# Optimization experiments

Measured on AMD Instinct MI355X. Metric: run time of the kernel, lower is better.

The kernel has to match this reference:

```python
import jax, jax.numpy as jnp
import numpy as np

HIDDEN = 2048
NUM_HEADS = 16
HEAD_DIM = HIDDEN // NUM_HEADS


def setup_inputs() -> dict:
    key = jax.random.key(0)
    k1, k2, k3 = jax.random.split(key, 3)
    B, S = 2, 2048
    hidden_states = jax.random.normal(k1, (B, S, HIDDEN), dtype=jnp.float32)
    attention_mask = jnp.zeros((B, 1, 1, S), dtype=jnp.float32)
    W_qkv = jax.random.normal(k2, (HIDDEN, 3 * HIDDEN), dtype=jnp.float32) * (1.0 / np.sqrt(HIDDEN))
    b_qkv = jnp.zeros((3 * HIDDEN,), dtype=jnp.float32)
    W_out = jax.random.normal(k3, (HIDDEN, HIDDEN), dtype=jnp.float32) * (1.0 / np.sqrt(HIDDEN))
    b_out = jnp.zeros((HIDDEN,), dtype=jnp.float32)
    return {"hidden_states": hidden_states, "attention_mask": attention_mask,
            "W_qkv": W_qkv, "b_qkv": b_qkv, "W_out": W_out, "b_out": b_out}


def reference(hidden_states, attention_mask, W_qkv, b_qkv, W_out, b_out):
    B, S, H = hidden_states.shape
    scale = 1.0 / np.sqrt(HEAD_DIM)
    # fused QKV projection (column-parallel linear, world_size=1)
    mixed = hidden_states @ W_qkv + b_qkv                      # [B,S,3H]
    q, k, v = jnp.split(mixed, 3, axis=-1)
    # [B, heads, S, head_dim]
    q = q.reshape(B, S, NUM_HEADS, HEAD_DIM).transpose(0, 2, 1, 3)
    k = k.reshape(B, S, NUM_HEADS, HEAD_DIM).transpose(0, 2, 1, 3)
    v = v.reshape(B, S, NUM_HEADS, HEAD_DIM).transpose(0, 2, 1, 3)
    scores = jnp.einsum('bhqd,bhkd->bhqk', q, k) * scale       # [B,h,S,S]
    scores = scores + attention_mask                            # additive mask broadcast
    probs = jax.nn.softmax(scores, axis=-1)
    ctx = jnp.einsum('bhqk,bhkd->bhqd', probs, v)               # [B,h,S,d]
    ctx = ctx.transpose(0, 2, 1, 3).reshape(B, S, H)
    return ctx @ W_out + b_out
```

## Files before the change

kernel.cpp:

```cpp
#include <hip/hip_runtime.h>
#include <hip/hip_bf16.h>
#include <stdint.h>

typedef __attribute__((ext_vector_type(4)))  float   f32x4;
typedef __attribute__((ext_vector_type(16))) float   f32x16;
typedef __attribute__((ext_vector_type(8)))  __bf16  bf16x8;
typedef __attribute__((ext_vector_type(8)))  short   s16x8;
typedef __attribute__((ext_vector_type(4)))  unsigned short u16x4;
typedef __attribute__((ext_vector_type(4)))  float   fl4;
typedef __attribute__((ext_vector_type(2)))  unsigned int u32x2;
typedef __attribute__((ext_vector_type(4)))  unsigned int u32x4;

#define DEVFN static __device__ __forceinline__

constexpr int BATCH = 2, SEQ = 2048, HID = 2048, NHEAD = 16, HDIM = 128;
constexpr int MROWS = BATCH * SEQ;
constexpr int N3    = 3 * HID;
constexpr float LOG2E = 1.44269504088896340736f;
constexpr float SCALE_LOG2E = 0.12751649736170852f;
constexpr float DEFER_THR = 11.541560327111708f;

DEVFN unsigned short f2bf(float f) {
  unsigned int u = __float_as_uint(f);
  u += 0x7FFFu + ((u >> 16) & 1u);
  return (unsigned short)(u >> 16);
}

DEVFN void async_cp16(const void* g, void* l) {
  __builtin_amdgcn_global_load_lds(
      (__attribute__((address_space(1))) void*)g,
      (__attribute__((address_space(3))) void*)l, 16, 0, 0);
}

DEVFN f32x4 mfma_bf16(bf16x8 a, bf16x8 b, f32x4 c) {
  return __builtin_amdgcn_mfma_f32_16x16x32_bf16(a, b, c, 0, 0, 0);
}
DEVFN f32x16 mfma32(bf16x8 a, bf16x8 b, f32x16 c) {
  return __builtin_amdgcn_mfma_f32_32x32x16_bf16(a, b, c, 0, 0, 0);
}
DEVFN unsigned cvt_pk_bf16(float lo, float hi) {
  unsigned r;
  asm("v_cvt_pk_bf16_f32 %0, %1, %2" : "=v"(r) : "v"(lo), "v"(hi));
  return r;
}

__global__ __launch_bounds__(256) void cvt_bf16(const float* __restrict__ x,
                                                unsigned short* __restrict__ hi, int n4) {
  for (int i = blockIdx.x * blockDim.x + threadIdx.x; i < n4; i += gridDim.x * blockDim.x) {
    fl4 v = ((const fl4*)x)[i];
    u16x4 h;
#pragma unroll
    for (int j = 0; j < 4; j++) h[j] = f2bf(v[j]);
    ((u16x4*)hi)[i] = h;
  }
}

__global__ __launch_bounds__(256) void cvt_transpose(const float* __restrict__ W,
                                                     unsigned short* __restrict__ T,
                                                     int R, int C) {
  __shared__ float tile[32][33];
  const int c0 = blockIdx.x * 32, r0 = blockIdx.y * 32;
  const int tx = threadIdx.x, ty = threadIdx.y;
#pragma unroll
  for (int i = 0; i < 4; i++) tile[ty + 8 * i][tx] = W[(size_t)(r0 + ty + 8 * i) * C + c0 + tx];
  __syncthreads();
#pragma unroll
  for (int i = 0; i < 4; i++) {
    const float v = tile[tx][ty + 8 * i];
    T[(size_t)(c0 + ty + 8 * i) * R + r0 + tx] = f2bf(v);
  }
}

template <bool OUT_BF16>
__global__ __launch_bounds__(512, 1) void gemm_ring(const unsigned short* __restrict__ A,
                                                    const unsigned short* __restrict__ Bt,
                                                    const float* __restrict__ bias,
                                                    void* __restrict__ Cout, int Ndim) {
  constexpr int KDIM  = 2048;
  constexpr int NT    = KDIM / 64;
  constexpr int ASLOT = 256 * 64;
  constexpr int BSLOT = 128 * 64;
  constexpr int SLOT  = ASLOT + BSLOT;
  __shared__ __align__(16) unsigned short smem[3 * SLOT];

  const int tid = threadIdx.x;
  const int wid = tid >> 6, lane = tid & 63;
  const int wm = wid >> 2, wn = wid & 3;
  const int g = lane >> 4, q = lane & 15;
  const int n0 = blockIdx.x * 128, m0 = blockIdx.y * 256;

  const int srow = (wid << 3) + (lane >> 3);
  const int scol = (((lane & 7) ^ (lane >> 3)) << 4);
  const char* gA = (const char*)A  + ((size_t)(m0 + srow) * KDIM) * 2 + scol;
  const char* gB = (const char*)Bt + ((size_t)(n0 + srow) * KDIM) * 2 + scol;
  const int dbase = ((wid << 3)) << 7;

  f32x4 acc[8][2] = {};
  const int axor = (q & 7) << 4;

  auto STAGE = [&](int tt, int slot) {
    char* sA = (char*)(smem + slot * SLOT);
    char* sB = (char*)(smem + slot * SLOT + ASLOT);
    const size_t koff = (size_t)tt << 7;
#pragma unroll
    for (int i = 0; i < 4; i++)
      async_cp16(gA + (size_t)(i * 64) * (KDIM * 2) + koff, sA + dbase + (i << 13));
#pragma unroll
    for (int i = 0; i < 2; i++)
      async_cp16(gB + (size_t)(i * 64) * (KDIM * 2) + koff, sB + dbase + (i << 13));
  };

  auto COMPUTE = [&](int slot) {
    const char* sA = (const char*)(smem + slot * SLOT);
    const char* sB = (const char*)(smem + slot * SLOT + ASLOT);
#pragma unroll
    for (int ks = 0; ks < 2; ks++) {
      const int kb = (ks << 6) + (g << 4);
      bf16x8 av[8], bv[2];
#pragma unroll
      for (int nf = 0; nf < 2; nf++) {
        const int row = (wn << 5) + (nf << 4) + q;
        bv[nf] = *(const bf16x8*)(sB + (row << 7) + (kb ^ axor));
      }
#pragma unroll
      for (int mf = 0; mf < 8; mf++) {
        const int row = (wm << 7) + (mf << 4) + q;
        av[mf] = *(const bf16x8*)(sA + (row << 7) + (kb ^ axor));
      }
#pragma unroll
      for (int mf = 0; mf < 8; mf++)
#pragma unroll
        for (int nf = 0; nf < 2; nf++)
          acc[mf][nf] = mfma_bf16(av[mf], bv[nf], acc[mf][nf]);
    }
  };

  STAGE(0, 0);
  STAGE(1, 1);
  int s2 = 2, sc = 0;
#pragma unroll 1
  for (int t = 0; t < NT - 2; ++t) {
    asm volatile("s_waitcnt vmcnt(6)" ::: "memory");
    __builtin_amdgcn_s_barrier();
    asm volatile("" ::: "memory");
    STAGE(t + 2, s2);
    COMPUTE(sc);
    s2 = (s2 == 2) ? 0 : s2 + 1;
    sc = (sc == 2) ? 0 : sc + 1;
  }
  asm volatile("s_waitcnt vmcnt(6)" ::: "memory");
  __builtin_amdgcn_s_barrier();
  asm volatile("" ::: "memory");
  COMPUTE(sc);
  sc = (sc == 2) ? 0 : sc + 1;
  asm volatile("s_waitcnt vmcnt(0)" ::: "memory");
  __builtin_amdgcn_s_barrier();
  asm volatile("" ::: "memory");
  COMPUTE(sc);

  float bvv[2];
#pragma unroll
  for (int nf = 0; nf < 2; nf++) bvv[nf] = bias[n0 + (wn << 5) + (nf << 4) + q];
#pragma unroll
  for (int mf = 0; mf < 8; mf++) {
    const int rowg = m0 + (wm << 7) + (mf << 4) + (g << 2);
#pragma unroll
    for (int nf = 0; nf < 2; nf++) {
      const int colg = n0 + (wn << 5) + (nf << 4) + q;
#pragma unroll
      for (int r = 0; r < 4; r++) {
        const float v = acc[mf][nf][r] + bvv[nf];
        if (OUT_BF16)
          ((unsigned short*)Cout)[(size_t)(rowg + r) * Ndim + colg] = f2bf(v);
        else
          ((float*)Cout)[(size_t)(rowg + r) * Ndim + colg] = v;
      }
    }
  }
}

__global__ __launch_bounds__(256) void transpose_v(const unsigned short* __restrict__ qkv,
                                                   unsigned short* __restrict__ vt) {
  __shared__ __align__(16) unsigned short tile[64][136];
  const int z = blockIdx.y, b = z >> 4, h = z & 15;
  const int s0 = blockIdx.x << 6;
  const int t = threadIdx.x;
#pragma unroll
  for (int i = 0; i < 4; i++) {
    const int idx = t + (i << 8);
    const int row = idx >> 4, ch = idx & 15;
    *(s16x8*)&tile[row][ch << 3] =
        *(const s16x8*)(qkv + (size_t)(b * SEQ + s0 + row) * N3 + 2 * HID + h * HDIM + (ch << 3));
  }
  __syncthreads();
#pragma unroll
  for (int i = 0; i < 4; i++) {
    const int idx = t + (i << 8);
    const int d = idx >> 3, sc = idx & 7;
    s16x8 v;
#pragma unroll
    for (int j = 0; j < 8; j++) v[j] = (short)tile[(sc << 3) + j][d];
    *(s16x8*)(vt + (size_t)(z * HDIM + d) * SEQ + s0 + (sc << 3)) = v;
  }
}

__global__ __launch_bounds__(256, 2) void attn_kernel(const unsigned short* __restrict__ qkv,
                                                      const unsigned short* __restrict__ vt,
                                                      const float* __restrict__ mask,
                                                      unsigned short* __restrict__ ctx) {
  constexpr int NT    = SEQ / 64;
  constexpr int KSLOT = 64 * 128;
  constexpr int VSLOT = 64 * 128;
  constexpr int SLOT  = KSLOT + VSLOT;
  __shared__ __align__(16) unsigned short sKV[2 * SLOT];
  __shared__ __align__(16) float sM[SEQ];

  const int bid = blockIdx.x;
  const int idx = bid >> 3;
  const int z  = ((bid & 7) << 2) + (idx >> 4);
  const int qb = idx & 15;
  const int b = z >> 4, h = z & 15;
  const int tid = threadIdx.x, wid = tid >> 6, lane = tid & 63;
  const int l31 = lane & 31, hi = lane >> 5;
  const int q0w = (qb << 7) + (wid << 5);

#pragma unroll
  for (int j = 0; j < 2; j++) {
    fl4 m = ((const fl4*)(mask + (size_t)b * SEQ))[tid + (j << 8)];
    m *= LOG2E;
    ((fl4*)sM)[tid + (j << 8)] = m;
  }

  bf16x8 bq[8];
  {
    const char* qrow = (const char*)(qkv + (size_t)(b * SEQ + q0w + l31) * N3 + h * HDIM);
#pragma unroll
    for (int kc = 0; kc < 8; kc++) bq[kc] = *(const bf16x8*)(qrow + (kc << 5) + (hi << 4));
  }

  f32x16 acc2[4] = {};
  float mrun = -1e30f, lrun = 0.f;

  const char* gK = (const char*)qkv + ((size_t)(b * SEQ) * N3 + HID + h * HDIM) * 2;
  const char* gV = (const char*)vt + ((size_t)z * HDIM * SEQ) * 2;

  auto STAGE = [&](int tt, int slot) {
    char* kb_ = (char*)(sKV + slot * SLOT);
    char* vb_ = kb_ + KSLOT * 2;
    const int k0 = tt << 6;
#pragma unroll
    for (int i = 0; i < 4; i++) {
      const int row = (i << 4) + (wid << 2) + (lane >> 4);
      const int sl  = lane & 15;
      const int dst = (i << 12) + (wid << 10);
      async_cp16(gK + ((size_t)(k0 + row) * N3) * 2 + (((sl ^ (row & 15))) << 4), kb_ + dst);
      const int sv  = sl ^ (row & 15);
      const int dhi = sv >> 3, kc8 = sv & 7;
      async_cp16(gV + ((size_t)((dhi << 6) + row) * SEQ + k0 + (kc8 << 3)) * 2, vb_ + dst);
    }
  };

  auto COMPUTE = [&](int t, int slot) {
    const char* sK = (const char*)(sKV + slot * SLOT);
    const char* sV = (const char*)(sKV + slot * SLOT + KSLOT);
    const int k0 = t << 6;

    f32x16 accs[2] = {};
    __builtin_amdgcn_s_setprio(1);
#pragma unroll
    for (int kb = 0; kb < 2; kb++)
#pragma unroll
      for (int kc = 0; kc < 8; kc++) {
        const int key = (kb << 5) + l31;
        const bf16x8 ka = *(const bf16x8*)(sK + (key << 8) +
                                           ((((kc << 1) + hi) ^ (l31 & 15)) << 4));
        accs[kb] = mfma32(ka, bq[kc], accs[kb]);
      }
    __builtin_amdgcn_s_setprio(0);

    float p_[2][16];
#pragma unroll
    for (int kb = 0; kb < 2; kb++) {
      fl4 mk[4];
#pragma unroll
      for (int m = 0; m < 4; m++) mk[m] = *(const fl4*)&sM[k0 + (kb << 5) + (m << 3) + (hi << 2)];
#pragma unroll
      for (int r = 0; r < 16; r++)
        p_[kb][r] = fmaf(accs[kb][r], SCALE_LOG2E, mk[r >> 2][r & 3]);
    }
    float mt = p_[0][0];
#pragma unroll
    for (int kb = 0; kb < 2; kb++)
#pragma unroll
      for (int r = 0; r < 16; r++) mt = fmaxf(mt, p_[kb][r]);
    mt = fmaxf(mt, __shfl_xor(mt, 32));
    if (!__all(mt <= mrun + DEFER_THR)) {
      const float mnew = fmaxf(mrun, mt);
      const float fs = exp2f(mrun - mnew);
      lrun *= fs;
#pragma unroll
      for (int r = 0; r < 16; r++) {
        const int qr = (r & 3) + ((r >> 2) << 3) + (hi << 2);
        const float fr = __shfl(fs, (lane & 32) | qr);
#pragma unroll
        for (int db = 0; db < 4; db++) acc2[db][r] *= fr;
      }
      mrun = mnew;
    }
    float ps = 0.f;
#pragma unroll
    for (int kb = 0; kb < 2; kb++)
#pragma unroll
      for (int r = 0; r < 16; r++) {
        const float e = exp2f(p_[kb][r] - mrun);
        p_[kb][r] = e;
        ps += e;
      }
    ps += __shfl_xor(ps, 32);
    lrun += ps;

    bf16x8 pa[4];
#pragma unroll
    for (int kb = 0; kb < 2; kb++)
#pragma unroll
      for (int hh = 0; hh < 2; hh++) {
        const float* pp = &p_[kb][hh << 3];
        const unsigned x01 = cvt_pk_bf16(pp[0], pp[1]);
        const unsigned x23 = cvt_pk_bf16(pp[2], pp[3]);
        const unsigned y01 = cvt_pk_bf16(pp[4], pp[5]);
        const unsigned y23 = cvt_pk_bf16(pp[6], pp[7]);
        const u32x2 sa = __builtin_amdgcn_permlane32_swap(x01, y01, false, false);
        const u32x2 sb = __builtin_amdgcn_permlane32_swap(x23, y23, false, false);
        const u32x4 w = {sa[0], sb[0], sa[1], sb[1]};
        pa[(kb << 1) + hh] = __builtin_bit_cast(bf16x8, w);
      }

    __builtin_amdgcn_s_setprio(1);
#pragma unroll
    for (int db = 0; db < 4; db++) {
      const int dd = ((db & 1) << 5) + l31;
#pragma unroll
      for (int ks = 0; ks < 4; ks++) {
        const int sv = ((db >> 1) << 3) + (ks << 1) + hi;
        const bf16x8 bv = *(const bf16x8*)(sV + (dd << 8) + ((sv ^ (l31 & 15)) << 4));
        acc2[db] = mfma32(pa[ks], bv, acc2[db]);
      }
    }
    __builtin_amdgcn_s_setprio(0);
  };

  STAGE(0, 0);
  __syncthreads();
#pragma unroll 1
  for (int t = 0; t < NT - 1; ++t) {
    STAGE(t + 1, (t + 1) & 1);
    COMPUTE(t, t & 1);
    asm volatile("s_waitcnt vmcnt(0)" ::: "memory");
    __builtin_amdgcn_s_barrier();
    asm volatile("" ::: "memory");
  }
  COMPUTE(NT - 1, (NT - 1) & 1);

  const float inv = 1.f / lrun;
#pragma unroll
  for (int r = 0; r < 16; r++) {
    const int qr = (r & 3) + ((r >> 2) << 3) + (hi << 2);
    const float fr = __shfl(inv, (lane & 32) | qr);
    unsigned short* crow = ctx + (size_t)(b * SEQ + q0w + qr) * HID + h * HDIM + l31;
#pragma unroll
    for (int db = 0; db < 4; db++) crow[db << 5] = f2bf(acc2[db][r] * fr);
  }
}

extern "C" void kernel_launch(void* const* d_in, const int* in_sizes, int n_in,
                              void* d_out, int out_size, void* d_ws, size_t ws_size,
                              hipStream_t stream) {
  const float* hs   = (const float*)d_in[0];
  const float* mask = (const float*)d_in[1];
  const float* Wqkv = (const float*)d_in[2];
  const float* bqkv = (const float*)d_in[3];
  const float* Wout = (const float*)d_in[4];
  const float* bout = (const float*)d_in[5];

  char* ws = (char*)d_ws;
  size_t off = 0;
  auto alloc = [&](size_t n) { char* p = ws + off; off += (n + 255) & ~(size_t)255; return p; };
  unsigned short* hs_bf = (unsigned short*)alloc((size_t)MROWS * HID * 2);
  unsigned short* wq_bf = (unsigned short*)alloc((size_t)N3 * HID * 2);
  unsigned short* wo_bf = (unsigned short*)alloc((size_t)HID * HID * 2);
  unsigned short* qkvb  = (unsigned short*)alloc((size_t)MROWS * N3 * 2);
  unsigned short* vtb   = (unsigned short*)alloc((size_t)BATCH * NHEAD * HDIM * SEQ * 2);
  unsigned short* ctxb  = (unsigned short*)alloc((size_t)MROWS * HID * 2);
  (void)ws_size;

  cvt_bf16<<<2048, 256, 0, stream>>>(hs, hs_bf, MROWS * HID / 4);
  dim3 tb(32, 8);
  cvt_transpose<<<dim3(N3 / 32, HID / 32), tb, 0, stream>>>(Wqkv, wq_bf, HID, N3);
  cvt_transpose<<<dim3(HID / 32, HID / 32), tb, 0, stream>>>(Wout, wo_bf, HID, HID);
  gemm_ring<true ><<<dim3(N3 / 128, MROWS / 256), 512, 0, stream>>>(hs_bf, wq_bf, bqkv, qkvb, N3);
  transpose_v<<<dim3(SEQ / 64, BATCH * NHEAD), 256, 0, stream>>>(qkvb, vtb);
  attn_kernel<<<512, 256, 0, stream>>>(qkvb, vtb, mask, ctxb);
  gemm_ring<false><<<dim3(HID / 128, MROWS / 256), 512, 0, stream>>>(ctxb, wo_bf, bout, (float*)d_out, HID);
}
```

Measured before the change: 265.2 us.

## Process two 32-row query sub-tiles per wave in attention to double K/V reuse

Each attention wave now handles 64 query rows as two independent 32-row sub-tiles. Each has its own online-softmax state and accumulators, and both share every K and V fragment read from LDS. The grid is halved and launch bounds drop to one block per CU to allow the larger register footprint. This cuts LDS traffic and K/V global loads per query, at the cost of lower occupancy and fewer blocks than CUs can comfortably absorb.

```diff
diff --git a/kernel.cpp b/kernel.cpp
--- a/kernel.cpp
+++ b/kernel.cpp
@@ -204,7 +204,7 @@
   }
 }
 
-__global__ __launch_bounds__(256, 2) void attn_kernel(const unsigned short* __restrict__ qkv,
+__global__ __launch_bounds__(256, 1) void attn_kernel(const unsigned short* __restrict__ qkv,
                                                       const unsigned short* __restrict__ vt,
                                                       const float* __restrict__ mask,
                                                       unsigned short* __restrict__ ctx) {
@@ -217,12 +217,12 @@
 
   const int bid = blockIdx.x;
   const int idx = bid >> 3;
-  const int z  = ((bid & 7) << 2) + (idx >> 4);
-  const int qb = idx & 15;
+  const int z  = ((bid & 7) << 2) + (idx >> 3);
+  const int qb = idx & 7;
   const int b = z >> 4, h = z & 15;
   const int tid = threadIdx.x, wid = tid >> 6, lane = tid & 63;
   const int l31 = lane & 31, hi = lane >> 5;
-  const int q0w = (qb << 7) + (wid << 5);
+  const int q0w = (qb << 8) + (wid << 6);
 
 #pragma unroll
   for (int j = 0; j < 2; j++) {
@@ -231,15 +231,16 @@
     ((fl4*)sM)[tid + (j << 8)] = m;
   }
 
-  bf16x8 bq[8];
-  {
-    const char* qrow = (const char*)(qkv + (size_t)(b * SEQ + q0w + l31) * N3 + h * HDIM);
-#pragma unroll
-    for (int kc = 0; kc < 8; kc++) bq[kc] = *(const bf16x8*)(qrow + (kc << 5) + (hi << 4));
-  }
-
-  f32x16 acc2[4] = {};
-  float mrun = -1e30f, lrun = 0.f;
+  bf16x8 bq[2][8];
+#pragma unroll
+  for (int qs = 0; qs < 2; qs++) {
+    const char* qrow = (const char*)(qkv + (size_t)(b * SEQ + q0w + (qs << 5) + l31) * N3 + h * HDIM);
+#pragma unroll
+    for (int kc = 0; kc < 8; kc++) bq[qs][kc] = *(const bf16x8*)(qrow + (kc << 5) + (hi << 4));
+  }
+
+  f32x16 acc2[2][4] = {};
+  float mrun[2] = {-1e30f, -1e30f}, lrun[2] = {0.f, 0.f};
 
   const char* gK = (const char*)qkv + ((size_t)(b * SEQ) * N3 + HID + h * HDIM) * 2;
   const char* gV = (const char*)vt + ((size_t)z * HDIM * SEQ) * 2;
@@ -265,7 +266,7 @@
     const char* sV = (const char*)(sKV + slot * SLOT + KSLOT);
     const int k0 = t << 6;
 
-    f32x16 accs[2] = {};
+    f32x16 accs[2][2] = {};
     __builtin_amdgcn_s_setprio(1);
 #pragma unroll
     for (int kb = 0; kb < 2; kb++)
@@ -274,66 +275,72 @@
         const int key = (kb << 5) + l31;
         const bf16x8 ka = *(const bf16x8*)(sK + (key << 8) +
                                            ((((kc << 1) + hi) ^ (l31 & 15)) << 4));
-        accs[kb] = mfma32(ka, bq[kc], accs[kb]);
+        accs[0][kb] = mfma32(ka, bq[0][kc], accs[0][kb]);
+        accs[1][kb] = mfma32(ka, bq[1][kc], accs[1][kb]);
       }
     __builtin_amdgcn_s_setprio(0);
 
-    float p_[2][16];
-#pragma unroll
-    for (int kb = 0; kb < 2; kb++) {
-      fl4 mk[4];
-#pragma unroll
-      for (int m = 0; m < 4; m++) mk[m] = *(const fl4*)&sM[k0 + (kb << 5) + (m << 3) + (hi << 2)];
-#pragma unroll
-      for (int r = 0; r < 16; r++)
-        p_[kb][r] = fmaf(accs[kb][r], SCALE_LOG2E, mk[r >> 2][r & 3]);
-    }
-    float mt = p_[0][0];
+    fl4 mk[2][4];
 #pragma unroll
     for (int kb = 0; kb < 2; kb++)
 #pragma unroll
-      for (int r = 0; r < 16; r++) mt = fmaxf(mt, p_[kb][r]);
-    mt = fmaxf(mt, __shfl_xor(mt, 32));
-    if (!__all(mt <= mrun + DEFER_THR)) {
-      const float mnew = fmaxf(mrun, mt);
-      const float fs = exp2f(mrun - mnew);
-      lrun *= fs;
-#pragma unroll
-      for (int r = 0; r < 16; r++) {
-        const int qr = (r & 3) + ((r >> 2) << 3) + (hi << 2);
-        const float fr = __shfl(fs, (lane & 32) | qr);
-#pragma unroll
-        for (int db = 0; db < 4; db++) acc2[db][r] *= fr;
-      }
-      mrun = mnew;
-    }
-    float ps = 0.f;
-#pragma unroll
-    for (int kb = 0; kb < 2; kb++)
-#pragma unroll
-      for (int r = 0; r < 16; r++) {
-        const float e = exp2f(p_[kb][r] - mrun);
-        p_[kb][r] = e;
-        ps += e;
-      }
-    ps += __shfl_xor(ps, 32);
-    lrun += ps;
-
-    bf16x8 pa[4];
-#pragma unroll
-    for (int kb = 0; kb < 2; kb++)
-#pragma unroll
-      for (int hh = 0; hh < 2; hh++) {
-        const float* pp = &p_[kb][hh << 3];
-        const unsigned x01 = cvt_pk_bf16(pp[0], pp[1]);
-        const unsigned x23 = cvt_pk_bf16(pp[2], pp[3]);
-        const unsigned y01 = cvt_pk_bf16(pp[4], pp[5]);
-        const unsigned y23 = cvt_pk_bf16(pp[6], pp[7]);
-        const u32x2 sa = __builtin_amdgcn_permlane32_swap(x01, y01, false, false);
-        const u32x2 sb = __builtin_amdgcn_permlane32_swap(x23, y23, false, false);
-        const u32x4 w = {sa[0], sb[0], sa[1], sb[1]};
-        pa[(kb << 1) + hh] = __builtin_bit_cast(bf16x8, w);
-      }
+      for (int m = 0; m < 4; m++) mk[kb][m] = *(const fl4*)&sM[k0 + (kb << 5) + (m << 3) + (hi << 2)];
+
+    bf16x8 pa[2][4];
+#pragma unroll
+    for (int qs = 0; qs < 2; qs++) {
+      float p_[2][16];
+#pragma unroll
+      for (int kb = 0; kb < 2; kb++)
+#pragma unroll
+        for (int r = 0; r < 16; r++)
+          p_[kb][r] = fmaf(accs[qs][kb][r], SCALE_LOG2E, mk[kb][r >> 2][r & 3]);
+      float mt = p_[0][0];
+#pragma unroll
+      for (int kb = 0; kb < 2; kb++)
+#pragma unroll
+        for (int r = 0; r < 16; r++) mt = fmaxf(mt, p_[kb][r]);
+      mt = fmaxf(mt, __shfl_xor(mt, 32));
+      if (!__all(mt <= mrun[qs] + DEFER_THR)) {
+        const float mnew = fmaxf(mrun[qs], mt);
+        const float fs = exp2f(mrun[qs] - mnew);
+        lrun[qs] *= fs;
+#pragma unroll
+        for (int r = 0; r < 16; r++) {
+          const int qr = (r & 3) + ((r >> 2) << 3) + (hi << 2);
+          const float fr = __shfl(fs, (lane & 32) | qr);
+#pragma unroll
+          for (int db = 0; db < 4; db++) acc2[qs][db][r] *= fr;
+        }
+        mrun[qs] = mnew;
+      }
+      float ps = 0.f;
+#pragma unroll
+      for (int kb = 0; kb < 2; kb++)
+#pragma unroll
+        for (int r = 0; r < 16; r++) {
+          const float e = exp2f(p_[kb][r] - mrun[qs]);
+          p_[kb][r] = e;
+          ps += e;
+        }
+      ps += __shfl_xor(ps, 32);
+      lrun[qs] += ps;
+
+#pragma unroll
+      for (int kb = 0; kb < 2; kb++)
+#pragma unroll
+        for (int hh = 0; hh < 2; hh++) {
+          const float* pp = &p_[kb][hh << 3];
+          const unsigned x01 = cvt_pk_bf16(pp[0], pp[1]);
+          const unsigned x23 = cvt_pk_bf16(pp[2], pp[3]);
+          const unsigned y01 = cvt_pk_bf16(pp[4], pp[5]);
+          const unsigned y23 = cvt_pk_bf16(pp[6], pp[7]);
+          const u32x2 sa = __builtin_amdgcn_permlane32_swap(x01, y01, false, false);
+          const u32x2 sb = __builtin_amdgcn_permlane32_swap(x23, y23, false, false);
+          const u32x4 w = {sa[0], sb[0], sa[1], sb[1]};
+          pa[qs][(kb << 1) + hh] = __builtin_bit_cast(bf16x8, w);
+        }
+    }
 
     __builtin_amdgcn_s_setprio(1);
 #pragma unroll
@@ -343,7 +350,8 @@
       for (int ks = 0; ks < 4; ks++) {
         const int sv = ((db >> 1) << 3) + (ks << 1) + hi;
         const bf16x8 bv = *(const bf16x8*)(sV + (dd << 8) + ((sv ^ (l31 & 15)) << 4));
-        acc2[db] = mfma32(pa[ks], bv, acc2[db]);
+        acc2[0][db] = mfma32(pa[0][ks], bv, acc2[0][db]);
+        acc2[1][db] = mfma32(pa[1][ks], bv, acc2[1][db]);
       }
     }
     __builtin_amdgcn_s_setprio(0);
@@ -361,14 +369,17 @@
   }
   COMPUTE(NT - 1, (NT - 1) & 1);
 
-  const float inv = 1.f / lrun;
-#pragma unroll
-  for (int r = 0; r < 16; r++) {
-    const int qr = (r & 3) + ((r >> 2) << 3) + (hi << 2);
-    const float fr = __shfl(inv, (lane & 32) | qr);
-    unsigned short* crow = ctx + (size_t)(b * SEQ + q0w + qr) * HID + h * HDIM + l31;
-#pragma unroll
-    for (int db = 0; db < 4; db++) crow[db << 5] = f2bf(acc2[db][r] * fr);
+#pragma unroll
+  for (int qs = 0; qs < 2; qs++) {
+    const float inv = 1.f / lrun[qs];
+#pragma unroll
+    for (int r = 0; r < 16; r++) {
+      const int qr = (r & 3) + ((r >> 2) << 3) + (hi << 2);
+      const float fr = __shfl(inv, (lane & 32) | qr);
+      unsigned short* crow = ctx + (size_t)(b * SEQ + q0w + (qs << 5) + qr) * HID + h * HDIM + l31;
+#pragma unroll
+      for (int db = 0; db < 4; db++) crow[db << 5] = f2bf(acc2[qs][db][r] * fr);
+    }
   }
 }
 
@@ -399,6 +410,6 @@
   cvt_transpose<<<dim3(HID / 32, HID / 32), tb, 0, stream>>>(Wout, wo_bf, HID, HID);
   gemm_ring<true ><<<dim3(N3 / 128, MROWS / 256), 512, 0, stream>>>(hs_bf, wq_bf, bqkv, qkvb, N3);
   transpose_v<<<dim3(SEQ / 64, BATCH * NHEAD), 256, 0, stream>>>(qkvb, vtb);
-  attn_kernel<<<512, 256, 0, stream>>>(qkvb, vtb, mask, ctxb);
+  attn_kernel<<<256, 256, 0, stream>>>(qkvb, vtb, mask, ctxb);
   gemm_ring<false><<<dim3(HID / 128, MROWS / 256), 512, 0, stream>>>(ctxb, wo_bf, bout, (float*)d_out, HID);
 }
```

Measured after the change: 292.6 us. 10.3% more time.
